# Kernel optimization log

Measured on AMD Instinct MI355X. Metric: run time of the kernel, lower is better.

The kernel has to match this reference:

```python
import jax, jax.numpy as jnp
import numpy as np

# Pauli-Z expectation table: sign of bit w in 4-bit index (wire 0 = MSB, axis order q0..q3)
_idx = np.arange(16)
_bits = (_idx[None, :] >> (3 - np.arange(4))[:, None]) & 1
_Z_TABLE = (1.0 - 2.0 * _bits).astype(np.float32)  # (4, 16)


def _apply_ry(state, theta, wire):
    # state: (N, 2,2,2,2) real amplitudes; RY = [[c,-s],[s,c]], c=cos(t/2), s=sin(t/2)
    ax = 1 + wire
    c = jnp.cos(theta / 2)
    s = jnp.sin(theta / 2)
    st = jnp.moveaxis(state, ax, 1)
    s0, s1 = st[:, 0], st[:, 1]
    st = jnp.stack([c * s0 - s * s1, s * s0 + c * s1], axis=1)
    return jnp.moveaxis(st, 1, ax)


def _apply_cnot(state, control, target):
    # flips the target axis on the control==1 slice (assumes target > control)
    ac, at = 1 + control, 1 + target
    s0 = jnp.take(state, 0, axis=ac)
    s1 = jnp.flip(jnp.take(state, 1, axis=ac), axis=at - 1)
    return jnp.stack([s0, s1], axis=ac)


def setup_inputs() -> dict:
    key = jax.random.key(0)
    ks = jax.random.split(key, 8)
    B = 8192
    x = jax.random.uniform(ks[0], (B, 1, 28, 28), dtype=jnp.float32)
    conv_w = jax.random.normal(ks[1], (4, 1, 2, 2), dtype=jnp.float32) * 0.5
    conv_b = jax.random.normal(ks[2], (4,), dtype=jnp.float32) * 0.1
    bn_gamma = jnp.ones((4,), jnp.float32)
    bn_beta = jnp.zeros((4,), jnp.float32)
    bn_mean = jnp.zeros((4,), jnp.float32)
    bn_var = jnp.ones((4,), jnp.float32)
    shortcut_weight = jnp.float32(1.0)
    theta = jax.random.normal(ks[3], (8,), dtype=jnp.float32)  # 8 trainable RY angles
    lin_w = jax.random.normal(ks[4], (10, 784), dtype=jnp.float32) * 0.03
    lin_b = jnp.zeros((10,), jnp.float32)
    log_scale = jnp.float32(1.0)
    return {"x": x, "conv_w": conv_w, "conv_b": conv_b, "bn_gamma": bn_gamma,
            "bn_beta": bn_beta, "bn_mean": bn_mean, "bn_var": bn_var,
            "shortcut_weight": shortcut_weight, "theta": theta,
            "lin_w": lin_w, "lin_b": lin_b, "log_scale": log_scale}


def reference(x, conv_w, conv_b, bn_gamma, bn_beta, bn_mean, bn_var,
              shortcut_weight, theta, lin_w, lin_b, log_scale):
    B = x.shape[0]
    # classical shortcut: conv(1->4, k2, s2) + BN (eval mode, running stats)
    sc = jax.lax.conv_general_dilated(
        x, conv_w, window_strides=(2, 2), padding='VALID',
        dimension_numbers=('NCHW', 'OIHW', 'NCHW')) + conv_b[None, :, None, None]
    sc = (sc - bn_mean[None, :, None, None]) * jax.lax.rsqrt(bn_var[None, :, None, None] + 1e-5)
    sc = sc * bn_gamma[None, :, None, None] + bn_beta[None, :, None, None]
    sc = sc.reshape(B, -1)  # (B, 784) channel-major, matches torch .view

    # extract 2x2 patches in (r, c) scan order -> (B*196, 4) with order [tl, tr, bl, br]
    img = x.reshape(B, 28, 28)
    patches = img.reshape(B, 14, 2, 14, 2).transpose(0, 1, 3, 2, 4).reshape(B * 196, 4)

    # RY encoding of |0000>: product state, amplitudes [cos(v/2), sin(v/2)] per wire
    half = patches * 0.5
    e = jnp.stack([jnp.cos(half), jnp.sin(half)], axis=-1)  # (N, 4, 2)
    state = jnp.einsum('na,nb,nc,nd->nabcd', e[:, 0], e[:, 1], e[:, 2], e[:, 3])

    # parameterized circuit: RY layer, CNOT(0,1), CNOT(2,3), RY layer
    for w in range(4):
        state = _apply_ry(state, theta[w], w)
    state = _apply_cnot(state, 0, 1)
    state = _apply_cnot(state, 2, 3)
    for w in range(4):
        state = _apply_ry(state, theta[4 + w], w)

    # <Z_w> expectations (real amplitudes -> probs = state**2)
    probs = (state ** 2).reshape(-1, 16)        # (B*196, 16)
    meas = probs @ jnp.asarray(_Z_TABLE).T      # (B*196, 4)
    qfeat = meas.reshape(B, 196 * 4)            # cat order: patch-major, wires inner

    feat = shortcut_weight * sc + qfeat
    logits = (feat @ lin_w.T + lin_b) * log_scale  # dropout is identity in eval
    return jax.nn.log_softmax(logits, axis=-1)
```

## Files before the change

kernel.cpp:

```cpp
#include <hip/hip_runtime.h>
#include <hip/hip_fp16.h>
#include <math.h>

#define BLOCK 256
#define WVS   4

typedef _Float16 h2v __attribute__((ext_vector_type(2)));

__device__ __forceinline__ float dot2h(unsigned a, unsigned b, float c) {
#if __has_builtin(__builtin_amdgcn_fdot2)
    return __builtin_amdgcn_fdot2(__builtin_bit_cast(h2v, a),
                                  __builtin_bit_cast(h2v, b), c, false);
#else
    h2v xa = __builtin_bit_cast(h2v, a), yb = __builtin_bit_cast(h2v, b);
    return c + (float)xa[0] * (float)yb[0] + (float)xa[1] * (float)yb[1];
#endif
}

__device__ __forceinline__ unsigned packh(float a, float b) {
    __half2 h = __float22half2_rn(make_float2(a, b));
    return __builtin_bit_cast(unsigned, h);
}

__device__ __forceinline__ unsigned pkadd(unsigned a, unsigned b) {
    __half2 r = __hadd2(__builtin_bit_cast(__half2, a), __builtin_bit_cast(__half2, b));
    return __builtin_bit_cast(unsigned, r);
}

template <int CTRL, int RMASK>
__device__ __forceinline__ float dppadd(float x) {
    int t = __builtin_amdgcn_update_dpp(0, __builtin_bit_cast(int, x),
                                        CTRL, RMASK, 0xf, false);
    return x + __builtin_bit_cast(float, t);
}
__device__ __forceinline__ float wave_sum64(float x) {
    x = dppadd<0x111, 0xf>(x);
    x = dppadd<0x112, 0xf>(x);
    x = dppadd<0x114, 0xf>(x);
    x = dppadd<0x118, 0xf>(x);
    x = dppadd<0x142, 0xa>(x);
    x = dppadd<0x143, 0xc>(x);
    return __builtin_bit_cast(float,
        __builtin_amdgcn_readlane(__builtin_bit_cast(int, x), 63));
}

__device__ __forceinline__ float sel10(const float L[10], int j) {
    float a0 = (j & 1) ? L[1] : L[0];
    float a2 = (j & 1) ? L[3] : L[2];
    float a4 = (j & 1) ? L[5] : L[4];
    float a6 = (j & 1) ? L[7] : L[6];
    float a8 = (j & 1) ? L[9] : L[8];
    float b0 = (j & 2) ? a2 : a0;
    float b4 = (j & 2) ? a6 : a4;
    float c0 = (j & 4) ? b4 : b0;
    return (j & 8) ? a8 : c0;
}

__global__ __launch_bounds__(BLOCK, 4) void quanv_fused4(
    const float* __restrict__ x,
    const float* __restrict__ conv_w,
    const float* __restrict__ conv_b,
    const float* __restrict__ bn_gamma,
    const float* __restrict__ bn_beta,
    const float* __restrict__ bn_mean,
    const float* __restrict__ bn_var,
    const float* __restrict__ sw_p,
    const float* __restrict__ theta,
    const float* __restrict__ lin_w,
    const float* __restrict__ lin_b,
    const float* __restrict__ log_scale_p,
    float* __restrict__ out)
{
    __shared__ __half lw[10 * 784];
    __shared__ __half fsc[WVS][2][784];

    const int t = threadIdx.x;
    const int lane = t & 63, wv = t >> 6;
    const int img0 = (blockIdx.x * WVS + wv) * 2;

    int off[4];
#pragma unroll
    for (int j = 0; j < 4; ++j) {
        int p = (j < 3) ? (lane + 64 * j) : (192 + (lane & 3));
        int i = p / 14, jj = p - i * 14;
        off[j] = i * 56 + jj * 2;
    }
    const float* xb0 = x + (size_t)img0 * 784;
    const float* xb1 = xb0 + 784;
    float2 pxa[4][2], pxb[4][2];
#pragma unroll
    for (int j = 0; j < 4; ++j) {
        pxa[j][0] = *(const float2*)(xb0 + off[j]);
        pxa[j][1] = *(const float2*)(xb0 + off[j] + 28);
        pxb[j][0] = *(const float2*)(xb1 + off[j]);
        pxb[j][1] = *(const float2*)(xb1 + off[j] + 28);
    }

    for (int q = t; q < 1960; q += BLOCK) {
        float4 v = *(const float4*)(lin_w + q * 4);
        int k = q / 196;
        int f = q * 4 - k * 784;
        uint2 pk;
        pk.x = packh(v.x, v.y);
        pk.y = packh(v.z, v.w);
        *(uint2*)&lw[k * 784 + f] = pk;
    }

    const float sw = sw_p[0], ls = log_scale_p[0];
    float wf[4][4], bf[4];
#pragma unroll
    for (int c = 0; c < 4; ++c) {
        float scale = bn_gamma[c] * rsqrtf(bn_var[c] + 1e-5f);
        float sws = sw * scale;
#pragma unroll
        for (int k = 0; k < 4; ++k) wf[c][k] = sws * conv_w[c * 4 + k];
        bf[c] = sw * (scale * (conv_b[c] - bn_mean[c]) + bn_beta[c]);
    }
    const float th0 = theta[0], th1 = theta[1], th2 = theta[2], th3 = theta[3];
    float sE0, cE0, sF0, cF0, sE1, cE1, sF1, cF1;
    __sincosf(theta[4], &sE0, &cE0);
    __sincosf(theta[5], &sF0, &cF0);
    __sincosf(theta[6], &sE1, &cE1);
    __sincosf(theta[7], &sF1, &cF1);

    auto qmeas = [&](float xa, float xbv, float tha, float thb,
                     float sE, float cE, float sF, float cF,
                     float& mA, float& mB) {
        float sa, ca, sb, cb;
        __sincosf(xa + tha, &sa, &ca);
        __sincosf(xbv + thb, &sb, &cb);
        mA = cE * ca - sE * (sa * sb);
        mB = cF * (ca * cb) - sF * sb;
    };

    unsigned qa[4][2], qb[4][2];
#pragma unroll
    for (int j = 0; j < 4; ++j) {
        if (j == 3 && lane >= 4) break;
        const int p = (j < 3) ? (lane + 64 * j) : (192 + lane);
        {
            float x00 = pxa[j][0].x, x01 = pxa[j][0].y;
            float x10 = pxa[j][1].x, x11 = pxa[j][1].y;
            float m0, m1, m2, m3;
            qmeas(x00, x01, th0, th1, sE0, cE0, sF0, cF0, m0, m1);
            qmeas(x10, x11, th2, th3, sE1, cE1, sF1, cF1, m2, m3);
            qa[j][0] = packh(m0, m1);
            qa[j][1] = packh(m2, m3);
#pragma unroll
            for (int c = 0; c < 4; ++c)
                fsc[wv][0][c * 196 + p] = __float2half(
                    wf[c][0] * x00 + wf[c][1] * x01 +
                    wf[c][2] * x10 + wf[c][3] * x11 + bf[c]);
        }
        {
            float x00 = pxb[j][0].x, x01 = pxb[j][0].y;
            float x10 = pxb[j][1].x, x11 = pxb[j][1].y;
            float m0, m1, m2, m3;
            qmeas(x00, x01, th0, th1, sE0, cE0, sF0, cF0, m0, m1);
            qmeas(x10, x11, th2, th3, sE1, cE1, sF1, cF1, m2, m3);
            qb[j][0] = packh(m0, m1);
            qb[j][1] = packh(m2, m3);
#pragma unroll
            for (int c = 0; c < 4; ++c)
                fsc[wv][1][c * 196 + p] = __float2half(
                    wf[c][0] * x00 + wf[c][1] * x01 +
                    wf[c][2] * x10 + wf[c][3] * x11 + bf[c]);
        }
    }

    __syncthreads();

    float acc0[10], acc1[10];
#pragma unroll
    for (int k = 0; k < 10; ++k) { acc0[k] = 0.f; acc1[k] = 0.f; }

#pragma unroll
    for (int j = 0; j < 4; ++j) {
        if (j == 3 && lane >= 4) break;
        const int p = (j < 3) ? (lane + 64 * j) : (192 + lane);
        uint2 f0 = *(uint2*)&fsc[wv][0][4 * p];
        uint2 f1 = *(uint2*)&fsc[wv][1][4 * p];
        const unsigned fa0 = pkadd(f0.x, qa[j][0]);
        const unsigned fa1 = pkadd(f0.y, qa[j][1]);
        const unsigned fb0 = pkadd(f1.x, qb[j][0]);
        const unsigned fb1 = pkadd(f1.y, qb[j][1]);
        const __half* wrow = &lw[4 * p];
#pragma unroll
        for (int k = 0; k < 10; ++k) {
            uint2 w = *(const uint2*)&wrow[k * 784];
            acc0[k] = dot2h(fa0, w.x, acc0[k]);
            acc0[k] = dot2h(fa1, w.y, acc0[k]);
            acc1[k] = dot2h(fb0, w.x, acc1[k]);
            acc1[k] = dot2h(fb1, w.y, acc1[k]);
        }
    }

    float L0[10], L1[10];
#pragma unroll
    for (int k = 0; k < 10; ++k) {
        L0[k] = wave_sum64(acc0[k]);
        L1[k] = wave_sum64(acc1[k]);
    }
#pragma unroll
    for (int k = 0; k < 10; ++k) {
        const float bk = lin_b[k];
        L0[k] = (L0[k] + bk) * ls;
        L1[k] = (L1[k] + bk) * ls;
    }

    float mA = L0[0], mB = L1[0];
#pragma unroll
    for (int k = 1; k < 10; ++k) { mA = fmaxf(mA, L0[k]); mB = fmaxf(mB, L1[k]); }
    float eA = 0.f, eB = 0.f;
#pragma unroll
    for (int k = 0; k < 10; ++k) {
        eA += __expf(L0[k] - mA);
        eB += __expf(L1[k] - mB);
    }
    const float lseA = mA + __logf(eA);
    const float lseB = mB + __logf(eB);

    const int j = lane & 15;
    if (lane < 10)
        out[(size_t)img0 * 10 + j] = sel10(L0, j) - lseA;
    else if (lane >= 16 && lane < 26)
        out[(size_t)(img0 + 1) * 10 + j] = sel10(L1, j) - lseB;
}

extern "C" void kernel_launch(void* const* d_in, const int* in_sizes, int n_in,
                              void* d_out, int out_size, void* d_ws, size_t ws_size,
                              hipStream_t stream) {
    const float* x         = (const float*)d_in[0];
    const float* conv_w    = (const float*)d_in[1];
    const float* conv_b    = (const float*)d_in[2];
    const float* bn_gamma  = (const float*)d_in[3];
    const float* bn_beta   = (const float*)d_in[4];
    const float* bn_mean   = (const float*)d_in[5];
    const float* bn_var    = (const float*)d_in[6];
    const float* sw        = (const float*)d_in[7];
    const float* theta     = (const float*)d_in[8];
    const float* lin_w     = (const float*)d_in[9];
    const float* lin_b     = (const float*)d_in[10];
    const float* log_scale = (const float*)d_in[11];
    float* out = (float*)d_out;

    const int B = in_sizes[0] / 784;
    dim3 grid(B / (WVS * 2)), block(BLOCK);
    hipLaunchKernelGGL(quanv_fused4, grid, block, 0, stream,
                       x, conv_w, conv_b, bn_gamma, bn_beta, bn_mean, bn_var,
                       sw, theta, lin_w, lin_b, log_scale, out);
}
```

Measured before the change: 21.74 us.

## Process one image per wave with 8-wave blocks, native sincos, paired-weight LDS layout

Each wave now handles a single image instead of two, and blocks grow to 512 threads with 8 waves, so the per-block lin_w fp16 staging covers the same number of images with fewer registers per thread. Sine and cosine are computed with the hardware sin/cos intrinsics on pre-scaled turns (fract then v_sin/v_cos) instead of __sincosf. The staged linear weights are interleaved in pairs of classes so each LDS read is a 16-byte load feeding two accumulators. Uniform scalars are forced into SGPRs with readfirstlane. The trade-off is more waves each doing redundant weight staging work per image, with lower per-wave ILP and less weight reuse across images.

```diff
diff --git a/kernel.cpp b/kernel.cpp
--- a/kernel.cpp
+++ b/kernel.cpp
@@ -2,8 +2,8 @@
 #include <hip/hip_fp16.h>
 #include <math.h>
 
-#define BLOCK 256
-#define WVS   4
+#define BLOCK 512
+#define WVS   8
 
 typedef _Float16 h2v __attribute__((ext_vector_type(2)));
 
@@ -25,6 +25,22 @@
 __device__ __forceinline__ unsigned pkadd(unsigned a, unsigned b) {
     __half2 r = __hadd2(__builtin_bit_cast(__half2, a), __builtin_bit_cast(__half2, b));
     return __builtin_bit_cast(unsigned, r);
+}
+
+__device__ __forceinline__ float rfl(float v) {
+    return __builtin_bit_cast(float,
+        __builtin_amdgcn_readfirstlane(__builtin_bit_cast(int, v)));
+}
+
+__device__ __forceinline__ void nsincos(float r, float& s, float& c) {
+#if __has_builtin(__builtin_amdgcn_sinf) && __has_builtin(__builtin_amdgcn_cosf) && __has_builtin(__builtin_amdgcn_fractf)
+    float rf = __builtin_amdgcn_fractf(r);
+    s = __builtin_amdgcn_sinf(rf);
+    c = __builtin_amdgcn_cosf(rf);
+#else
+    float rf = r - floorf(r);
+    __sincosf(rf * 6.2831853071795864f, &s, &c);
+#endif
 }
 
 template <int CTRL, int RMASK>
@@ -56,7 +72,7 @@
     return (j & 8) ? a8 : c0;
 }
 
-__global__ __launch_bounds__(BLOCK, 4) void quanv_fused4(
+__global__ __launch_bounds__(BLOCK, 8) void quanv_fused6(
     const float* __restrict__ x,
     const float* __restrict__ conv_w,
     const float* __restrict__ conv_b,
@@ -71,160 +87,125 @@
     const float* __restrict__ log_scale_p,
     float* __restrict__ out)
 {
-    __shared__ __half lw[10 * 784];
-    __shared__ __half fsc[WVS][2][784];
+    __shared__ __half lw2[5 * 196 * 8];
+    __shared__ __half fsc[WVS][784];
 
     const int t = threadIdx.x;
     const int lane = t & 63, wv = t >> 6;
-    const int img0 = (blockIdx.x * WVS + wv) * 2;
-
-    int off[4];
+    const int img = blockIdx.x * WVS + wv;
+    const float INV2PI = 0.15915494309189535f;
+
+    const float* xb = x + (size_t)img * 784;
+    float2 px[4][2];
 #pragma unroll
     for (int j = 0; j < 4; ++j) {
         int p = (j < 3) ? (lane + 64 * j) : (192 + (lane & 3));
         int i = p / 14, jj = p - i * 14;
-        off[j] = i * 56 + jj * 2;
-    }
-    const float* xb0 = x + (size_t)img0 * 784;
-    const float* xb1 = xb0 + 784;
-    float2 pxa[4][2], pxb[4][2];
-#pragma unroll
-    for (int j = 0; j < 4; ++j) {
-        pxa[j][0] = *(const float2*)(xb0 + off[j]);
-        pxa[j][1] = *(const float2*)(xb0 + off[j] + 28);
-        pxb[j][0] = *(const float2*)(xb1 + off[j]);
-        pxb[j][1] = *(const float2*)(xb1 + off[j] + 28);
+        const int off = i * 56 + jj * 2;
+        px[j][0] = *(const float2*)(xb + off);
+        px[j][1] = *(const float2*)(xb + off + 28);
     }
 
     for (int q = t; q < 1960; q += BLOCK) {
         float4 v = *(const float4*)(lin_w + q * 4);
         int k = q / 196;
-        int f = q * 4 - k * 784;
+        int p = q - k * 196;
         uint2 pk;
         pk.x = packh(v.x, v.y);
         pk.y = packh(v.z, v.w);
-        *(uint2*)&lw[k * 784 + f] = pk;
-    }
-
-    const float sw = sw_p[0], ls = log_scale_p[0];
-    float wf[4][4], bf[4];
+        *(uint2*)&lw2[(k >> 1) * 1568 + p * 8 + (k & 1) * 4] = pk;
+    }
+
+    const float sw = sw_p[0];
+    const float ls = rfl(log_scale_p[0]);
+    float wfS[16], bfS[4];
 #pragma unroll
     for (int c = 0; c < 4; ++c) {
         float scale = bn_gamma[c] * rsqrtf(bn_var[c] + 1e-5f);
         float sws = sw * scale;
 #pragma unroll
-        for (int k = 0; k < 4; ++k) wf[c][k] = sws * conv_w[c * 4 + k];
-        bf[c] = sw * (scale * (conv_b[c] - bn_mean[c]) + bn_beta[c]);
-    }
-    const float th0 = theta[0], th1 = theta[1], th2 = theta[2], th3 = theta[3];
+        for (int k = 0; k < 4; ++k) wfS[c * 4 + k] = rfl(sws * conv_w[c * 4 + k]);
+        bfS[c] = rfl(sw * (scale * (conv_b[c] - bn_mean[c]) + bn_beta[c]));
+    }
+    float thc[4];
+#pragma unroll
+    for (int w = 0; w < 4; ++w) thc[w] = rfl(theta[w] * INV2PI);
     float sE0, cE0, sF0, cF0, sE1, cE1, sF1, cF1;
-    __sincosf(theta[4], &sE0, &cE0);
-    __sincosf(theta[5], &sF0, &cF0);
-    __sincosf(theta[6], &sE1, &cE1);
-    __sincosf(theta[7], &sF1, &cF1);
-
-    auto qmeas = [&](float xa, float xbv, float tha, float thb,
-                     float sE, float cE, float sF, float cF,
-                     float& mA, float& mB) {
-        float sa, ca, sb, cb;
-        __sincosf(xa + tha, &sa, &ca);
-        __sincosf(xbv + thb, &sb, &cb);
-        mA = cE * ca - sE * (sa * sb);
-        mB = cF * (ca * cb) - sF * sb;
-    };
-
-    unsigned qa[4][2], qb[4][2];
+    {
+        float s, c;
+        nsincos(theta[4] * INV2PI, s, c); sE0 = rfl(s); cE0 = rfl(c);
+        nsincos(theta[5] * INV2PI, s, c); sF0 = rfl(s); cF0 = rfl(c);
+        nsincos(theta[6] * INV2PI, s, c); sE1 = rfl(s); cE1 = rfl(c);
+        nsincos(theta[7] * INV2PI, s, c); sF1 = rfl(s); cF1 = rfl(c);
+    }
+
+    unsigned qr[4][2];
 #pragma unroll
     for (int j = 0; j < 4; ++j) {
         if (j == 3 && lane >= 4) break;
         const int p = (j < 3) ? (lane + 64 * j) : (192 + lane);
-        {
-            float x00 = pxa[j][0].x, x01 = pxa[j][0].y;
-            float x10 = pxa[j][1].x, x11 = pxa[j][1].y;
-            float m0, m1, m2, m3;
-            qmeas(x00, x01, th0, th1, sE0, cE0, sF0, cF0, m0, m1);
-            qmeas(x10, x11, th2, th3, sE1, cE1, sF1, cF1, m2, m3);
-            qa[j][0] = packh(m0, m1);
-            qa[j][1] = packh(m2, m3);
-#pragma unroll
-            for (int c = 0; c < 4; ++c)
-                fsc[wv][0][c * 196 + p] = __float2half(
-                    wf[c][0] * x00 + wf[c][1] * x01 +
-                    wf[c][2] * x10 + wf[c][3] * x11 + bf[c]);
+        const float x00 = px[j][0].x, x01 = px[j][0].y;
+        const float x10 = px[j][1].x, x11 = px[j][1].y;
+        float sa, ca, sb, cb;
+        nsincos(fmaf(x00, INV2PI, thc[0]), sa, ca);
+        nsincos(fmaf(x01, INV2PI, thc[1]), sb, cb);
+        const float m0 = cE0 * ca - sE0 * (sa * sb);
+        const float m1 = cF0 * (ca * cb) - sF0 * sb;
+        nsincos(fmaf(x10, INV2PI, thc[2]), sa, ca);
+        nsincos(fmaf(x11, INV2PI, thc[3]), sb, cb);
+        const float m2 = cE1 * ca - sE1 * (sa * sb);
+        const float m3 = cF1 * (ca * cb) - sF1 * sb;
+        qr[j][0] = packh(m0, m1);
+        qr[j][1] = packh(m2, m3);
+#pragma unroll
+        for (int c = 0; c < 4; ++c) {
+            float v = fmaf(wfS[c * 4 + 0], x00,
+                      fmaf(wfS[c * 4 + 1], x01,
+                      fmaf(wfS[c * 4 + 2], x10,
+                      fmaf(wfS[c * 4 + 3], x11, bfS[c]))));
+            fsc[wv][c * 196 + p] = __float2half(v);
         }
-        {
-            float x00 = pxb[j][0].x, x01 = pxb[j][0].y;
-            float x10 = pxb[j][1].x, x11 = pxb[j][1].y;
-            float m0, m1, m2, m3;
-            qmeas(x00, x01, th0, th1, sE0, cE0, sF0, cF0, m0, m1);
-            qmeas(x10, x11, th2, th3, sE1, cE1, sF1, cF1, m2, m3);
-            qb[j][0] = packh(m0, m1);
-            qb[j][1] = packh(m2, m3);
-#pragma unroll
-            for (int c = 0; c < 4; ++c)
-                fsc[wv][1][c * 196 + p] = __float2half(
-                    wf[c][0] * x00 + wf[c][1] * x01 +
-                    wf[c][2] * x10 + wf[c][3] * x11 + bf[c]);
-        }
     }
 
     __syncthreads();
 
-    float acc0[10], acc1[10];
-#pragma unroll
-    for (int k = 0; k < 10; ++k) { acc0[k] = 0.f; acc1[k] = 0.f; }
+    float acc[10];
+#pragma unroll
+    for (int k = 0; k < 10; ++k) acc[k] = 0.f;
 
 #pragma unroll
     for (int j = 0; j < 4; ++j) {
         if (j == 3 && lane >= 4) break;
         const int p = (j < 3) ? (lane + 64 * j) : (192 + lane);
-        uint2 f0 = *(uint2*)&fsc[wv][0][4 * p];
-        uint2 f1 = *(uint2*)&fsc[wv][1][4 * p];
-        const unsigned fa0 = pkadd(f0.x, qa[j][0]);
-        const unsigned fa1 = pkadd(f0.y, qa[j][1]);
-        const unsigned fb0 = pkadd(f1.x, qb[j][0]);
-        const unsigned fb1 = pkadd(f1.y, qb[j][1]);
-        const __half* wrow = &lw[4 * p];
-#pragma unroll
-        for (int k = 0; k < 10; ++k) {
-            uint2 w = *(const uint2*)&wrow[k * 784];
-            acc0[k] = dot2h(fa0, w.x, acc0[k]);
-            acc0[k] = dot2h(fa1, w.y, acc0[k]);
-            acc1[k] = dot2h(fb0, w.x, acc1[k]);
-            acc1[k] = dot2h(fb1, w.y, acc1[k]);
+        uint2 f = *(const uint2*)&fsc[wv][4 * p];
+        const unsigned fa0 = pkadd(f.x, qr[j][0]);
+        const unsigned fa1 = pkadd(f.y, qr[j][1]);
+        const __half* wbase = &lw2[p * 8];
+#pragma unroll
+        for (int kk = 0; kk < 5; ++kk) {
+            uint4 w = *(const uint4*)&wbase[kk * 1568];
+            acc[2 * kk]     = dot2h(fa0, w.x, acc[2 * kk]);
+            acc[2 * kk]     = dot2h(fa1, w.y, acc[2 * kk]);
+            acc[2 * kk + 1] = dot2h(fa0, w.z, acc[2 * kk + 1]);
+            acc[2 * kk + 1] = dot2h(fa1, w.w, acc[2 * kk + 1]);
         }
     }
 
-    float L0[10], L1[10];
-#pragma unroll
-    for (int k = 0; k < 10; ++k) {
-        L0[k] = wave_sum64(acc0[k]);
-        L1[k] = wave_sum64(acc1[k]);
-    }
-#pragma unroll
-    for (int k = 0; k < 10; ++k) {
-        const float bk = lin_b[k];
-        L0[k] = (L0[k] + bk) * ls;
-        L1[k] = (L1[k] + bk) * ls;
-    }
-
-    float mA = L0[0], mB = L1[0];
-#pragma unroll
-    for (int k = 1; k < 10; ++k) { mA = fmaxf(mA, L0[k]); mB = fmaxf(mB, L1[k]); }
-    float eA = 0.f, eB = 0.f;
-#pragma unroll
-    for (int k = 0; k < 10; ++k) {
-        eA += __expf(L0[k] - mA);
-        eB += __expf(L1[k] - mB);
-    }
-    const float lseA = mA + __logf(eA);
-    const float lseB = mB + __logf(eB);
-
-    const int j = lane & 15;
+    float L[10];
+#pragma unroll
+    for (int k = 0; k < 10; ++k)
+        L[k] = (wave_sum64(acc[k]) + lin_b[k]) * ls;
+
+    float m = L[0];
+#pragma unroll
+    for (int k = 1; k < 10; ++k) m = fmaxf(m, L[k]);
+    float e = 0.f;
+#pragma unroll
+    for (int k = 0; k < 10; ++k) e += __expf(L[k] - m);
+    const float lse = m + __logf(e);
+
     if (lane < 10)
-        out[(size_t)img0 * 10 + j] = sel10(L0, j) - lseA;
-    else if (lane >= 16 && lane < 26)
-        out[(size_t)(img0 + 1) * 10 + j] = sel10(L1, j) - lseB;
+        out[(size_t)img * 10 + lane] = sel10(L, lane) - lse;
 }
 
 extern "C" void kernel_launch(void* const* d_in, const int* in_sizes, int n_in,
@@ -245,8 +226,8 @@
     float* out = (float*)d_out;
 
     const int B = in_sizes[0] / 784;
-    dim3 grid(B / (WVS * 2)), block(BLOCK);
-    hipLaunchKernelGGL(quanv_fused4, grid, block, 0, stream,
+    dim3 grid(B / WVS), block(BLOCK);
+    hipLaunchKernelGGL(quanv_fused6, grid, block, 0, stream,
                        x, conv_w, conv_b, bn_gamma, bn_beta, bn_mean, bn_var,
                        sw, theta, lin_w, lin_b, log_scale, out);
 }
```

Measured after the change: 21.18 us. 2.6% less time.
